# Performance work log

Measured on AMD Instinct MI355X. Metric: run time of the kernel, lower is better.

The kernel has to match this reference:

```python
import jax, jax.numpy as jnp
import numpy as np

B, S, D_MODEL = 2, 2048, 1024
HEADS = 16
DK = D_MODEL // HEADS  # 64
Q_RANK, RANK = 6, 2
ROPE_BASE = 10000.0


def _xavier(key, shape):
    # torch nn.init.xavier_uniform_ on weight (out,in); stored here as (in,out)
    fan_in, fan_out = shape
    a = (6.0 / (fan_in + fan_out)) ** 0.5
    return jax.random.uniform(key, shape, jnp.float32, -a, a)


def setup_inputs() -> dict:
    key = jax.random.key(0)
    ks = jax.random.split(key, 10)
    inp = {
        "q": jax.random.normal(ks[0], (B, S, D_MODEL), jnp.float32),
        "k": jax.random.normal(ks[1], (B, S, D_MODEL), jnp.float32),
        "v": jax.random.normal(ks[2], (B, S, D_MODEL), jnp.float32),
        # causal mask; mask==0 -> -inf in scores
        "mask": jnp.tril(jnp.ones((S, S), dtype=bool))[None, None],
        "W_Aq": _xavier(ks[3], (D_MODEL, Q_RANK * HEADS)),
        "W_Ak": _xavier(ks[4], (D_MODEL, RANK * HEADS)),
        "W_Av": _xavier(ks[5], (D_MODEL, RANK * HEADS)),
        "W_Bq": _xavier(ks[6], (D_MODEL, Q_RANK * DK)),
        "W_Bk": _xavier(ks[7], (D_MODEL, RANK * DK)),
        "W_Bv": _xavier(ks[8], (D_MODEL, RANK * DK)),
        "Wo": _xavier(ks[9], (D_MODEL, D_MODEL)),
    }
    return inp


def _rotary_cos_sin(seq_len, dim):
    inv_freq = 1.0 / (ROPE_BASE ** (jnp.arange(0, dim, 2, dtype=jnp.float32) / dim))
    freqs = jnp.outer(jnp.arange(seq_len, dtype=jnp.float32), inv_freq)  # [S, dim/2]
    return jnp.cos(freqs)[None, :, None, :], jnp.sin(freqs)[None, :, None, :]


def _apply_rotary(x, cos, sin):
    # x: [B, S, R, dk]; rotate-half style RoPE
    d = x.shape[-1] // 2
    x1, x2 = x[..., :d], x[..., d:]
    return jnp.concatenate([x1 * cos + x2 * sin, -x1 * sin + x2 * cos], axis=-1)


def reference(q, k, v, mask, W_Aq, W_Ak, W_Av, W_Bq, W_Bk, W_Bv, Wo):
    Bn, Sn, D = q.shape
    # low-rank factor projections
    A_q = (q @ W_Aq).reshape(Bn, Sn, HEADS, Q_RANK)
    A_k = (k @ W_Ak).reshape(Bn, Sn, HEADS, RANK)
    A_v = (v @ W_Av).reshape(Bn, Sn, HEADS, RANK)
    B_q = (q @ W_Bq).reshape(Bn, Sn, Q_RANK, DK)
    B_k = (k @ W_Bk).reshape(Bn, Sn, RANK, DK)
    B_v = (v @ W_Bv).reshape(Bn, Sn, RANK, DK)
    cos, sin = _rotary_cos_sin(Sn, DK)
    B_q = _apply_rotary(B_q, cos, sin)
    B_k = _apply_rotary(B_k, cos, sin)
    # reconstruct per-head q/k/v: [B,H,S,dk]
    qh = jnp.einsum("bshr,bsrd->bhsd", A_q, B_q) / Q_RANK
    kh = jnp.einsum("bshr,bsrd->bhsd", A_k, B_k) / RANK
    vh = jnp.einsum("bshr,bsrd->bhsd", A_v, B_v) / RANK
    # NOTE: original divides by d_k (not sqrt(d_k)) -- faithful to source
    score = jnp.einsum("bhqd,bhkd->bhqk", qh, kh) / DK
    score = jnp.where(mask, score, -jnp.inf)
    # dropout is identity (eval / dropout=0.0)
    att = jax.nn.softmax(score, axis=-1)
    out = jnp.einsum("bhqk,bhkd->bqhd", att, vh).reshape(Bn, Sn, D)
    return out @ Wo
```

## Files before the change

kernel.cpp:

```cpp
#include <hip/hip_runtime.h>
#include <hip/hip_bf16.h>


typedef __attribute__((ext_vector_type(8))) short short8;
typedef __attribute__((ext_vector_type(4))) float floatx4;

#define MFMA16(a, b, c) __builtin_amdgcn_mfma_f32_16x16x32_bf16(a, b, c, 0, 0, 0)

__device__ __forceinline__ unsigned short bfbits(float x) {
    __hip_bfloat16 h = __float2bfloat16(x);
    return *(unsigned short*)&h;
}

__device__ __forceinline__ float wsrc(int n, int k,
                                      const float* __restrict__ Aq, const float* __restrict__ Bq,
                                      const float* __restrict__ Ak, const float* __restrict__ Bk,
                                      const float* __restrict__ Av, const float* __restrict__ Bv,
                                      const float* __restrict__ Wo) {
    if (n < 96) return Aq[(size_t)k * 96 + n];
    if (n < 480) return Bq[(size_t)k * 384 + (n - 96)];
    if (n < 512) return 0.f;
    if (n < 544) return Ak[(size_t)k * 32 + (n - 512)];
    if (n < 672) return Bk[(size_t)k * 128 + (n - 544)];
    if (n < 768) return 0.f;
    if (n < 800) return Av[(size_t)k * 32 + (n - 768)];
    if (n < 928) return Bv[(size_t)k * 128 + (n - 800)];
    if (n < 1024) return 0.f;
    return Wo[(size_t)k * 1024 + (n - 1024)];
}

__global__ __launch_bounds__(256) void pack_wT_kernel(const float* __restrict__ Aq,
                                                      const float* __restrict__ Bq,
                                                      const float* __restrict__ Ak,
                                                      const float* __restrict__ Bk,
                                                      const float* __restrict__ Av,
                                                      const float* __restrict__ Bv,
                                                      const float* __restrict__ Wo,
                                                      __hip_bfloat16* __restrict__ outBase) {
    __shared__ float tile[64][65];
    int k0 = blockIdx.x * 64, n0 = blockIdx.y * 64;
    int tid = threadIdx.x;
#pragma unroll
    for (int p = 0; p < 16; ++p) {
        int idx = p * 256 + tid;
        int kl = idx >> 6, nl = idx & 63;
        tile[kl][nl] = wsrc(n0 + nl, k0 + kl, Aq, Bq, Ak, Bk, Av, Bv, Wo);
    }
    __syncthreads();
#pragma unroll
    for (int p = 0; p < 16; ++p) {
        int idx = p * 256 + tid;
        int nl = idx >> 6, kl = idx & 63;
        outBase[(size_t)(n0 + nl) * 1024 + k0 + kl] = __float2bfloat16(tile[kl][nl]);
    }
}

__global__ __launch_bounds__(256) void gemm3_kernel(const float* __restrict__ q,
                                                    const float* __restrict__ k,
                                                    const float* __restrict__ v,
                                                    const __hip_bfloat16* __restrict__ WT,
                                                    float* __restrict__ Pq,
                                                    float* __restrict__ Pk,
                                                    float* __restrict__ Pv) {
    __shared__ __align__(16) __hip_bfloat16 As[128][72];
    __shared__ __align__(16) __hip_bfloat16 Bs[64][72];
    int t = blockIdx.x;
    const float* A; float* C; int N, n0, wrow;
    if (t < 8)       { A = q; C = Pq; N = 512; n0 = t * 64;        wrow = t * 64; }
    else if (t < 12) { A = k; C = Pk; N = 256; n0 = (t - 8) * 64;  wrow = 512 + (t - 8) * 64; }
    else             { A = v; C = Pv; N = 256; n0 = (t - 12) * 64; wrow = 768 + (t - 12) * 64; }
    int m0 = blockIdx.y * 128;
    int tid = threadIdx.x;
    int wave = tid >> 6, lane = tid & 63, quad = lane >> 4, l15 = lane & 15;
    int wm = wave >> 1, wn = wave & 1;
    floatx4 acc[4][2];
#pragma unroll
    for (int mt = 0; mt < 4; ++mt)
#pragma unroll
        for (int nt = 0; nt < 2; ++nt) acc[mt][nt] = (floatx4){0.f, 0.f, 0.f, 0.f};

    for (int k0 = 0; k0 < 1024; k0 += 64) {
#pragma unroll
        for (int pp = 0; pp < 8; ++pp) {
            int idx = pp * 256 + tid;
            int row = idx >> 4, c4 = (idx & 15) * 4;
            float4 av = *(const float4*)(A + (size_t)(m0 + row) * 1024 + k0 + c4);
            ushort4 bv;
            bv.x = bfbits(av.x); bv.y = bfbits(av.y); bv.z = bfbits(av.z); bv.w = bfbits(av.w);
            *(ushort4*)&As[row][c4] = bv;
        }
#pragma unroll
        for (int pp = 0; pp < 2; ++pp) {
            int idx = pp * 256 + tid;
            int row = idx >> 3, c8 = (idx & 7) * 8;
            *(uint4*)&Bs[row][c8] = *(const uint4*)(WT + (size_t)(wrow + row) * 1024 + k0 + c8);
        }
        __syncthreads();
#pragma unroll
        for (int ks = 0; ks < 64; ks += 32) {
            short8 af[4], bf[2];
#pragma unroll
            for (int t2 = 0; t2 < 4; ++t2)
                af[t2] = *(const short8*)&As[wm * 64 + t2 * 16 + l15][ks + quad * 8];
#pragma unroll
            for (int t2 = 0; t2 < 2; ++t2)
                bf[t2] = *(const short8*)&Bs[wn * 32 + t2 * 16 + l15][ks + quad * 8];
#pragma unroll
            for (int mt = 0; mt < 4; ++mt)
#pragma unroll
                for (int nt = 0; nt < 2; ++nt)
                    acc[mt][nt] = MFMA16(af[mt], bf[nt], acc[mt][nt]);
        }
        __syncthreads();
    }
#pragma unroll
    for (int mt = 0; mt < 4; ++mt)
#pragma unroll
        for (int nt = 0; nt < 2; ++nt)
#pragma unroll
            for (int r = 0; r < 4; ++r) {
                int row = m0 + wm * 64 + mt * 16 + quad * 4 + r;
                int col = n0 + wn * 32 + nt * 16 + l15;
                C[(size_t)row * N + col] = acc[mt][nt][r];
            }
}

__global__ __launch_bounds__(256) void gemm_out_kernel(const __hip_bfloat16* __restrict__ A,
                                                       const __hip_bfloat16* __restrict__ BT,
                                                       float* __restrict__ C) {
    __shared__ __align__(16) __hip_bfloat16 As[128][72];
    __shared__ __align__(16) __hip_bfloat16 Bs[64][72];
    int n0 = blockIdx.x * 64, m0 = blockIdx.y * 128;
    int tid = threadIdx.x;
    int wave = tid >> 6, lane = tid & 63, quad = lane >> 4, l15 = lane & 15;
    int wm = wave >> 1, wn = wave & 1;
    floatx4 acc[4][2];
#pragma unroll
    for (int mt = 0; mt < 4; ++mt)
#pragma unroll
        for (int nt = 0; nt < 2; ++nt) acc[mt][nt] = (floatx4){0.f, 0.f, 0.f, 0.f};

    for (int k0 = 0; k0 < 1024; k0 += 64) {
#pragma unroll
        for (int pp = 0; pp < 4; ++pp) {
            int idx = pp * 256 + tid;
            int row = idx >> 3, c8 = (idx & 7) * 8;
            *(uint4*)&As[row][c8] = *(const uint4*)(A + (size_t)(m0 + row) * 1024 + k0 + c8);
        }
#pragma unroll
        for (int pp = 0; pp < 2; ++pp) {
            int idx = pp * 256 + tid;
            int row = idx >> 3, c8 = (idx & 7) * 8;
            *(uint4*)&Bs[row][c8] = *(const uint4*)(BT + (size_t)(n0 + row) * 1024 + k0 + c8);
        }
        __syncthreads();
#pragma unroll
        for (int ks = 0; ks < 64; ks += 32) {
            short8 af[4], bf[2];
#pragma unroll
            for (int t2 = 0; t2 < 4; ++t2)
                af[t2] = *(const short8*)&As[wm * 64 + t2 * 16 + l15][ks + quad * 8];
#pragma unroll
            for (int t2 = 0; t2 < 2; ++t2)
                bf[t2] = *(const short8*)&Bs[wn * 32 + t2 * 16 + l15][ks + quad * 8];
#pragma unroll
            for (int mt = 0; mt < 4; ++mt)
#pragma unroll
                for (int nt = 0; nt < 2; ++nt)
                    acc[mt][nt] = MFMA16(af[mt], bf[nt], acc[mt][nt]);
        }
        __syncthreads();
    }
#pragma unroll
    for (int mt = 0; mt < 4; ++mt)
#pragma unroll
        for (int nt = 0; nt < 2; ++nt)
#pragma unroll
            for (int r = 0; r < 4; ++r) {
                int row = m0 + wm * 64 + mt * 16 + quad * 4 + r;
                int col = n0 + wn * 32 + nt * 16 + l15;
                C[(size_t)row * 1024 + col] = acc[mt][nt][r];
            }
}

__global__ __launch_bounds__(256) void combine_rope_kernel(const float* __restrict__ Pq,
                                                           const float* __restrict__ Pk,
                                                           const float* __restrict__ Pv,
                                                           __hip_bfloat16* __restrict__ qh,
                                                           __hip_bfloat16* __restrict__ kh,
                                                           __hip_bfloat16* __restrict__ vh) {
    int t = blockIdx.x, tid = threadIdx.x;
    int b = t >> 11, s = t & 2047;
    __shared__ float Lq[512], Lk[256], Lv[256];
    for (int i = tid; i < 512; i += 256) Lq[i] = Pq[(size_t)t * 512 + i];
    Lk[tid] = Pk[(size_t)t * 256 + tid];
    Lv[tid] = Pv[(size_t)t * 256 + tid];
    __syncthreads();
    if (tid < 192) {
        int r = tid >> 5, d = tid & 31;
        float inv = __expf(-(float)d * 0.28782313662425576f);
        float rev = (float)s * inv * 0.15915494309189535f;
        rev -= floorf(rev);
        float sn = __builtin_amdgcn_sinf(rev);
        float cs = __builtin_amdgcn_cosf(rev);
        float x1 = Lq[96 + r * 64 + d], x2 = Lq[96 + r * 64 + d + 32];
        Lq[96 + r * 64 + d] = x1 * cs + x2 * sn;
        Lq[96 + r * 64 + d + 32] = -x1 * sn + x2 * cs;
    } else {
        int i2 = tid - 192;
        int r = i2 >> 5, d = i2 & 31;
        float inv = __expf(-(float)d * 0.28782313662425576f);
        float rev = (float)s * inv * 0.15915494309189535f;
        rev -= floorf(rev);
        float sn = __builtin_amdgcn_sinf(rev);
        float cs = __builtin_amdgcn_cosf(rev);
        float x1 = Lk[32 + r * 64 + d], x2 = Lk[32 + r * 64 + d + 32];
        Lk[32 + r * 64 + d] = x1 * cs + x2 * sn;
        Lk[32 + r * 64 + d + 32] = -x1 * sn + x2 * cs;
    }
    __syncthreads();
    const float QSCALE = 1.4426950408889634f / 768.0f;
    int bh0 = b * 16;
    for (int i = tid; i < 1024; i += 256) {
        int h = i >> 6, d = i & 63;
        float aq = 0.f;
#pragma unroll
        for (int r = 0; r < 6; ++r) aq += Lq[h * 6 + r] * Lq[96 + r * 64 + d];
        size_t o = ((size_t)(bh0 + h) * 2048 + s) * 64 + d;
        qh[o] = __float2bfloat16(aq * QSCALE);
        float ak = Lk[h * 2] * Lk[32 + d] + Lk[h * 2 + 1] * Lk[96 + d];
        kh[o] = __float2bfloat16(ak);
        float av = Lv[h * 2] * Lv[32 + d] + Lv[h * 2 + 1] * Lv[96 + d];
        vh[o] = __float2bfloat16(av * 0.5f);
    }
}

__global__ __launch_bounds__(256) void transpose_v_kernel(const __hip_bfloat16* __restrict__ vh,
                                                          __hip_bfloat16* __restrict__ vT) {
    __shared__ __hip_bfloat16 tile[64][65];
    int s0 = blockIdx.x * 64, bh = blockIdx.y;
    int tid = threadIdx.x;
#pragma unroll
    for (int p = 0; p < 16; ++p) {
        int idx = p * 256 + tid;
        int r = idx >> 6, c = idx & 63;
        tile[r][c] = vh[((size_t)bh * 2048 + s0 + r) * 64 + c];
    }
    __syncthreads();
#pragma unroll
    for (int p = 0; p < 16; ++p) {
        int idx = p * 256 + tid;
        int r = idx >> 6, c = idx & 63;
        vT[((size_t)bh * 64 + r) * 2048 + s0 + c] = tile[c][r];
    }
}

__global__ __launch_bounds__(256) void flash_kernel(const __hip_bfloat16* __restrict__ qh,
                                                    const __hip_bfloat16* __restrict__ kh,
                                                    const __hip_bfloat16* __restrict__ vT,
                                                    __hip_bfloat16* __restrict__ att) {
    int lin = blockIdx.x + (blockIdx.y << 4);
    int bh = ((lin & 7) << 2) | ((lin >> 3) & 3);
    int p = 15 - (lin >> 5);
    int tid = threadIdx.x;
    int wave = tid >> 6, lane = tid & 63, quad = lane >> 4, l15 = lane & 15;
    int q0 = p * 128;
    __shared__ __align__(16) __hip_bfloat16 Ks[64][72];
    __shared__ __align__(16) __hip_bfloat16 Vts[64][72];
    __shared__ __align__(16) __hip_bfloat16 Ps[4][32][72];

    short8 aq[2][2];
#pragma unroll
    for (int m = 0; m < 2; ++m) {
        const __hip_bfloat16* qrow =
            qh + ((size_t)bh * 2048 + q0 + wave * 32 + m * 16 + l15) * 64 + quad * 8;
        aq[m][0] = *(const short8*)(qrow);
        aq[m][1] = *(const short8*)(qrow + 32);
    }

    floatx4 o[2][4];
#pragma unroll
    for (int m = 0; m < 2; ++m)
#pragma unroll
        for (int nt = 0; nt < 4; ++nt) o[m][nt] = (floatx4){0.f, 0.f, 0.f, 0.f};
    float rs[2][4] = {{0.f, 0.f, 0.f, 0.f}, {0.f, 0.f, 0.f, 0.f}};

    int jmax = 2 * p + 1;
    for (int j = 0; j <= jmax; ++j) {
        int k0 = j * 64;
#pragma unroll
        for (int pp = 0; pp < 2; ++pp) {
            int idx = pp * 256 + tid;
            int row = idx >> 3, c8 = (idx & 7) * 8;
            *(uint4*)&Ks[row][c8] = *(const uint4*)(kh + ((size_t)bh * 2048 + k0 + row) * 64 + c8);
            *(uint4*)&Vts[row][c8] = *(const uint4*)(vT + ((size_t)bh * 64 + row) * 2048 + k0 + c8);
        }
        __syncthreads();

        int krel = j - 2 * p;
        bool skip0 = (krel == 1) && (wave * 32 < 64);
        bool skip1 = (krel == 1) && (wave * 32 + 16 < 64);

        floatx4 s[2][4];
#pragma unroll
        for (int m = 0; m < 2; ++m)
#pragma unroll
            for (int nt = 0; nt < 4; ++nt) s[m][nt] = (floatx4){0.f, 0.f, 0.f, 0.f};
#pragma unroll
        for (int nt = 0; nt < 4; ++nt) {
            short8 bk0 = *(const short8*)&Ks[nt * 16 + l15][quad * 8];
            short8 bk1 = *(const short8*)&Ks[nt * 16 + l15][32 + quad * 8];
            if (!skip0) {
                s[0][nt] = MFMA16(aq[0][0], bk0, s[0][nt]);
                s[0][nt] = MFMA16(aq[0][1], bk1, s[0][nt]);
            }
            if (!skip1) {
                s[1][nt] = MFMA16(aq[1][0], bk0, s[1][nt]);
                s[1][nt] = MFMA16(aq[1][1], bk1, s[1][nt]);
            }
        }
#pragma unroll
        for (int m = 0; m < 2; ++m) {
            bool skip = m == 0 ? skip0 : skip1;
            if (skip) continue;
            int sbase = wave * 32 + m * 16;
            bool domask = (krel >= 0) && (krel * 64 + 63 > sbase);
            if (domask) {
#pragma unroll
                for (int nt = 0; nt < 4; ++nt) {
                    int kcol = k0 + nt * 16 + l15;
#pragma unroll
                    for (int r = 0; r < 4; ++r)
                        if (kcol > q0 + sbase + quad * 4 + r) s[m][nt][r] = -__builtin_inff();
                }
            }
#pragma unroll
            for (int nt = 0; nt < 4; ++nt)
#pragma unroll
                for (int r = 0; r < 4; ++r) {
                    float pe = exp2f(s[m][nt][r]);
                    rs[m][r] += pe;
                    Ps[wave][m * 16 + quad * 4 + r][nt * 16 + l15] = __float2bfloat16(pe);
                }
        }
        __builtin_amdgcn_s_waitcnt(0xC07F);
        short8 pa[2][2];
#pragma unroll
        for (int m = 0; m < 2; ++m) {
            pa[m][0] = *(const short8*)&Ps[wave][m * 16 + l15][quad * 8];
            pa[m][1] = *(const short8*)&Ps[wave][m * 16 + l15][32 + quad * 8];
        }
#pragma unroll
        for (int nt = 0; nt < 4; ++nt) {
            short8 bv0 = *(const short8*)&Vts[nt * 16 + l15][quad * 8];
            short8 bv1 = *(const short8*)&Vts[nt * 16 + l15][32 + quad * 8];
            if (!skip0) {
                o[0][nt] = MFMA16(pa[0][0], bv0, o[0][nt]);
                o[0][nt] = MFMA16(pa[0][1], bv1, o[0][nt]);
            }
            if (!skip1) {
                o[1][nt] = MFMA16(pa[1][0], bv0, o[1][nt]);
                o[1][nt] = MFMA16(pa[1][1], bv1, o[1][nt]);
            }
        }
        __syncthreads();
    }
    int b = bh >> 4, h = bh & 15;
#pragma unroll
    for (int m = 0; m < 2; ++m) {
        float l_i[4];
#pragma unroll
        for (int r = 0; r < 4; ++r) {
            float x = rs[m][r];
            x += __shfl_xor(x, 1, 64);
            x += __shfl_xor(x, 2, 64);
            x += __shfl_xor(x, 4, 64);
            x += __shfl_xor(x, 8, 64);
            l_i[r] = x;
        }
        size_t obase = ((size_t)b * 2048 + q0 + wave * 32 + m * 16 + quad * 4) * 1024 + h * 64;
#pragma unroll
        for (int nt = 0; nt < 4; ++nt)
#pragma unroll
            for (int r = 0; r < 4; ++r)
                att[obase + (size_t)r * 1024 + nt * 16 + l15] = __float2bfloat16(o[m][nt][r] / l_i[r]);
    }
}

extern "C" void kernel_launch(void* const* d_in, const int* in_sizes, int n_in,
                              void* d_out, int out_size, void* d_ws, size_t ws_size,
                              hipStream_t stream) {
    const float* q = (const float*)d_in[0];
    const float* k = (const float*)d_in[1];
    const float* v = (const float*)d_in[2];
    const float* W_Aq = (const float*)d_in[4];
    const float* W_Ak = (const float*)d_in[5];
    const float* W_Av = (const float*)d_in[6];
    const float* W_Bq = (const float*)d_in[7];
    const float* W_Bk = (const float*)d_in[8];
    const float* W_Bv = (const float*)d_in[9];
    const float* Wo = (const float*)d_in[10];
    float* out = (float*)d_out;

    char* w = (char*)d_ws;
    __hip_bfloat16* qh = (__hip_bfloat16*)(w + 0);
    __hip_bfloat16* khp = (__hip_bfloat16*)(w + 8388608);
    __hip_bfloat16* vhN = (__hip_bfloat16*)(w + 16777216);
    __hip_bfloat16* WT = (__hip_bfloat16*)(w + 25165824);
    __hip_bfloat16* WoT = (__hip_bfloat16*)(w + 27262976);
    float* Pq = (float*)(w + 29360128);
    float* Pk = (float*)(w + 37748736);
    float* Pv = (float*)(w + 41943040);
    __hip_bfloat16* att = (__hip_bfloat16*)(w + 29360128);
    __hip_bfloat16* vT = (__hip_bfloat16*)(w + 37748736);

    pack_wT_kernel<<<dim3(16, 32), 256, 0, stream>>>(W_Aq, W_Bq, W_Ak, W_Bk, W_Av, W_Bv, Wo, WT);
    gemm3_kernel<<<dim3(16, 32), 256, 0, stream>>>(q, k, v, WT, Pq, Pk, Pv);
    combine_rope_kernel<<<4096, 256, 0, stream>>>(Pq, Pk, Pv, qh, khp, vhN);
    transpose_v_kernel<<<dim3(32, 32), 256, 0, stream>>>(vhN, vT);
    flash_kernel<<<dim3(16, 32), 256, 0, stream>>>(qh, khp, vT, att);
    gemm_out_kernel<<<dim3(16, 32), 256, 0, stream>>>(att, WoT, out);
}
```

Before: 260.0 us.

## Rework pipeline: larger GEMM tiles, bf16 intermediates, fused combine+transpose, leaner flash

Both GEMMs now use 128x128 tiles on a 1D grid with grouped block ordering, and the projection GEMM writes bf16 instead of fp32 intermediates. The combine/RoPE and V-transpose kernels are merged into one kernel that handles 16 tokens per block and writes vT directly. The flash kernel moves to 64-row query tiles, prefetches the next K/V tile into registers, and computes row sums with an MFMA against a ones matrix instead of shuffles. These changes aim to cut intermediate memory traffic and launch count and to improve load balance, at the cost of extra bf16 rounding in the intermediates and fewer blocks (256) in the GEMMs.

```diff
diff --git a/kernel.cpp b/kernel.cpp
--- a/kernel.cpp
+++ b/kernel.cpp
@@ -7,9 +7,13 @@
 
 #define MFMA16(a, b, c) __builtin_amdgcn_mfma_f32_16x16x32_bf16(a, b, c, 0, 0, 0)
 
+__device__ __forceinline__ float b2f(short s) {
+    unsigned int u = ((unsigned int)(unsigned short)s) << 16;
+    float f; __builtin_memcpy(&f, &u, 4); return f;
+}
 __device__ __forceinline__ unsigned short bfbits(float x) {
     __hip_bfloat16 h = __float2bfloat16(x);
-    return *(unsigned short*)&h;
+    unsigned short u; __builtin_memcpy(&u, &h, 2); return u;
 }
 
 __device__ __forceinline__ float wsrc(int n, int k,
@@ -59,25 +63,26 @@
                                                     const float* __restrict__ k,
                                                     const float* __restrict__ v,
                                                     const __hip_bfloat16* __restrict__ WT,
-                                                    float* __restrict__ Pq,
-                                                    float* __restrict__ Pk,
-                                                    float* __restrict__ Pv) {
+                                                    __hip_bfloat16* __restrict__ Pq,
+                                                    __hip_bfloat16* __restrict__ Pk,
+                                                    __hip_bfloat16* __restrict__ Pv) {
     __shared__ __align__(16) __hip_bfloat16 As[128][72];
-    __shared__ __align__(16) __hip_bfloat16 Bs[64][72];
-    int t = blockIdx.x;
-    const float* A; float* C; int N, n0, wrow;
-    if (t < 8)       { A = q; C = Pq; N = 512; n0 = t * 64;        wrow = t * 64; }
-    else if (t < 12) { A = k; C = Pk; N = 256; n0 = (t - 8) * 64;  wrow = 512 + (t - 8) * 64; }
-    else             { A = v; C = Pv; N = 256; n0 = (t - 12) * 64; wrow = 768 + (t - 12) * 64; }
-    int m0 = blockIdx.y * 128;
+    __shared__ __align__(16) __hip_bfloat16 Bs[128][72];
+    int lin = blockIdx.x;
+    int t = (lin >> 3) & 7;
+    int m0 = ((lin & 7) + ((lin >> 6) << 3)) * 128;
+    const float* A; __hip_bfloat16* C; int N, n0, wrow;
+    if (t < 4)      { A = q; C = Pq; N = 512; n0 = t * 128;        wrow = t * 128; }
+    else if (t < 6) { A = k; C = Pk; N = 256; n0 = (t - 4) * 128;  wrow = 512 + (t - 4) * 128; }
+    else            { A = v; C = Pv; N = 256; n0 = (t - 6) * 128;  wrow = 768 + (t - 6) * 128; }
     int tid = threadIdx.x;
     int wave = tid >> 6, lane = tid & 63, quad = lane >> 4, l15 = lane & 15;
     int wm = wave >> 1, wn = wave & 1;
-    floatx4 acc[4][2];
+    floatx4 acc[4][4];
 #pragma unroll
     for (int mt = 0; mt < 4; ++mt)
 #pragma unroll
-        for (int nt = 0; nt < 2; ++nt) acc[mt][nt] = (floatx4){0.f, 0.f, 0.f, 0.f};
+        for (int nt = 0; nt < 4; ++nt) acc[mt][nt] = (floatx4){0.f, 0.f, 0.f, 0.f};
 
     for (int k0 = 0; k0 < 1024; k0 += 64) {
 #pragma unroll
@@ -90,7 +95,7 @@
             *(ushort4*)&As[row][c4] = bv;
         }
 #pragma unroll
-        for (int pp = 0; pp < 2; ++pp) {
+        for (int pp = 0; pp < 4; ++pp) {
             int idx = pp * 256 + tid;
             int row = idx >> 3, c8 = (idx & 7) * 8;
             *(uint4*)&Bs[row][c8] = *(const uint4*)(WT + (size_t)(wrow + row) * 1024 + k0 + c8);
@@ -98,17 +103,16 @@
         __syncthreads();
 #pragma unroll
         for (int ks = 0; ks < 64; ks += 32) {
-            short8 af[4], bf[2];
-#pragma unroll
-            for (int t2 = 0; t2 < 4; ++t2)
+            short8 af[4], bf[4];
+#pragma unroll
+            for (int t2 = 0; t2 < 4; ++t2) {
                 af[t2] = *(const short8*)&As[wm * 64 + t2 * 16 + l15][ks + quad * 8];
-#pragma unroll
-            for (int t2 = 0; t2 < 2; ++t2)
-                bf[t2] = *(const short8*)&Bs[wn * 32 + t2 * 16 + l15][ks + quad * 8];
+                bf[t2] = *(const short8*)&Bs[wn * 64 + t2 * 16 + l15][ks + quad * 8];
+            }
 #pragma unroll
             for (int mt = 0; mt < 4; ++mt)
 #pragma unroll
-                for (int nt = 0; nt < 2; ++nt)
+                for (int nt = 0; nt < 4; ++nt)
                     acc[mt][nt] = MFMA16(af[mt], bf[nt], acc[mt][nt]);
         }
         __syncthreads();
@@ -116,12 +120,12 @@
 #pragma unroll
     for (int mt = 0; mt < 4; ++mt)
 #pragma unroll
-        for (int nt = 0; nt < 2; ++nt)
+        for (int nt = 0; nt < 4; ++nt)
 #pragma unroll
             for (int r = 0; r < 4; ++r) {
                 int row = m0 + wm * 64 + mt * 16 + quad * 4 + r;
-                int col = n0 + wn * 32 + nt * 16 + l15;
-                C[(size_t)row * N + col] = acc[mt][nt][r];
+                int col = n0 + wn * 64 + nt * 16 + l15;
+                C[(size_t)row * N + col] = __float2bfloat16(acc[mt][nt][r]);
             }
 }
 
@@ -129,16 +133,18 @@
                                                        const __hip_bfloat16* __restrict__ BT,
                                                        float* __restrict__ C) {
     __shared__ __align__(16) __hip_bfloat16 As[128][72];
-    __shared__ __align__(16) __hip_bfloat16 Bs[64][72];
-    int n0 = blockIdx.x * 64, m0 = blockIdx.y * 128;
+    __shared__ __align__(16) __hip_bfloat16 Bs[128][72];
+    int lin = blockIdx.x;
+    int n0 = ((lin >> 3) & 7) * 128;
+    int m0 = ((lin & 7) + ((lin >> 6) << 3)) * 128;
     int tid = threadIdx.x;
     int wave = tid >> 6, lane = tid & 63, quad = lane >> 4, l15 = lane & 15;
     int wm = wave >> 1, wn = wave & 1;
-    floatx4 acc[4][2];
+    floatx4 acc[4][4];
 #pragma unroll
     for (int mt = 0; mt < 4; ++mt)
 #pragma unroll
-        for (int nt = 0; nt < 2; ++nt) acc[mt][nt] = (floatx4){0.f, 0.f, 0.f, 0.f};
+        for (int nt = 0; nt < 4; ++nt) acc[mt][nt] = (floatx4){0.f, 0.f, 0.f, 0.f};
 
     for (int k0 = 0; k0 < 1024; k0 += 64) {
 #pragma unroll
@@ -146,27 +152,21 @@
             int idx = pp * 256 + tid;
             int row = idx >> 3, c8 = (idx & 7) * 8;
             *(uint4*)&As[row][c8] = *(const uint4*)(A + (size_t)(m0 + row) * 1024 + k0 + c8);
-        }
-#pragma unroll
-        for (int pp = 0; pp < 2; ++pp) {
-            int idx = pp * 256 + tid;
-            int row = idx >> 3, c8 = (idx & 7) * 8;
             *(uint4*)&Bs[row][c8] = *(const uint4*)(BT + (size_t)(n0 + row) * 1024 + k0 + c8);
         }
         __syncthreads();
 #pragma unroll
         for (int ks = 0; ks < 64; ks += 32) {
-            short8 af[4], bf[2];
-#pragma unroll
-            for (int t2 = 0; t2 < 4; ++t2)
+            short8 af[4], bf[4];
+#pragma unroll
+            for (int t2 = 0; t2 < 4; ++t2) {
                 af[t2] = *(const short8*)&As[wm * 64 + t2 * 16 + l15][ks + quad * 8];
-#pragma unroll
-            for (int t2 = 0; t2 < 2; ++t2)
-                bf[t2] = *(const short8*)&Bs[wn * 32 + t2 * 16 + l15][ks + quad * 8];
+                bf[t2] = *(const short8*)&Bs[wn * 64 + t2 * 16 + l15][ks + quad * 8];
+            }
 #pragma unroll
             for (int mt = 0; mt < 4; ++mt)
 #pragma unroll
-                for (int nt = 0; nt < 2; ++nt)
+                for (int nt = 0; nt < 4; ++nt)
                     acc[mt][nt] = MFMA16(af[mt], bf[nt], acc[mt][nt]);
         }
         __syncthreads();
@@ -174,84 +174,110 @@
 #pragma unroll
     for (int mt = 0; mt < 4; ++mt)
 #pragma unroll
-        for (int nt = 0; nt < 2; ++nt)
+        for (int nt = 0; nt < 4; ++nt)
 #pragma unroll
             for (int r = 0; r < 4; ++r) {
                 int row = m0 + wm * 64 + mt * 16 + quad * 4 + r;
-                int col = n0 + wn * 32 + nt * 16 + l15;
+                int col = n0 + wn * 64 + nt * 16 + l15;
                 C[(size_t)row * 1024 + col] = acc[mt][nt][r];
             }
 }
 
-__global__ __launch_bounds__(256) void combine_rope_kernel(const float* __restrict__ Pq,
-                                                           const float* __restrict__ Pk,
-                                                           const float* __restrict__ Pv,
-                                                           __hip_bfloat16* __restrict__ qh,
-                                                           __hip_bfloat16* __restrict__ kh,
-                                                           __hip_bfloat16* __restrict__ vh) {
-    int t = blockIdx.x, tid = threadIdx.x;
-    int b = t >> 11, s = t & 2047;
-    __shared__ float Lq[512], Lk[256], Lv[256];
-    for (int i = tid; i < 512; i += 256) Lq[i] = Pq[(size_t)t * 512 + i];
-    Lk[tid] = Pk[(size_t)t * 256 + tid];
-    Lv[tid] = Pv[(size_t)t * 256 + tid];
+__global__ __launch_bounds__(256) void combine_vt_kernel(const __hip_bfloat16* __restrict__ Pq,
+                                                         const __hip_bfloat16* __restrict__ Pk,
+                                                         const __hip_bfloat16* __restrict__ Pv,
+                                                         __hip_bfloat16* __restrict__ qh,
+                                                         __hip_bfloat16* __restrict__ kh,
+                                                         __hip_bfloat16* __restrict__ vT) {
+    __shared__ __align__(16) __hip_bfloat16 LAq[16][96];
+    __shared__ __align__(16) __hip_bfloat16 LAk[16][32];
+    __shared__ __align__(16) __hip_bfloat16 LAv[16][32];
+    __shared__ __align__(16) __hip_bfloat16 LBq[16][6][72];
+    __shared__ __align__(16) __hip_bfloat16 LBk[16][2][72];
+    __shared__ __align__(16) __hip_bfloat16 LBv[16][2][72];
+    int tid = threadIdx.x;
+    int token0 = blockIdx.x * 16;
+    int b = token0 >> 11, s0 = token0 & 2047, bh0 = b * 16;
+
+    for (int i = tid; i < 16 * 512; i += 256) {
+        int s = i >> 9, c = i & 511;
+        __hip_bfloat16 val = Pq[(size_t)(token0 + s) * 512 + c];
+        if (c < 96) LAq[s][c] = val;
+        else if (c < 480) LBq[s][(c - 96) >> 6][(c - 96) & 63] = val;
+    }
+    for (int i = tid; i < 16 * 256; i += 256) {
+        int s = i >> 8, c = i & 255;
+        __hip_bfloat16 vk = Pk[(size_t)(token0 + s) * 256 + c];
+        __hip_bfloat16 vv = Pv[(size_t)(token0 + s) * 256 + c];
+        if (c < 32) { LAk[s][c] = vk; LAv[s][c] = vv; }
+        else if (c < 160) {
+            LBk[s][(c - 32) >> 6][(c - 32) & 63] = vk;
+            LBv[s][(c - 32) >> 6][(c - 32) & 63] = vv;
+        }
+    }
     __syncthreads();
-    if (tid < 192) {
-        int r = tid >> 5, d = tid & 31;
+    for (int i = tid; i < 4096; i += 256) {
+        int s = i >> 8, rr = (i >> 5) & 7, d = i & 31;
         float inv = __expf(-(float)d * 0.28782313662425576f);
-        float rev = (float)s * inv * 0.15915494309189535f;
+        float rev = (float)(s0 + s) * inv * 0.15915494309189535f;
         rev -= floorf(rev);
         float sn = __builtin_amdgcn_sinf(rev);
         float cs = __builtin_amdgcn_cosf(rev);
-        float x1 = Lq[96 + r * 64 + d], x2 = Lq[96 + r * 64 + d + 32];
-        Lq[96 + r * 64 + d] = x1 * cs + x2 * sn;
-        Lq[96 + r * 64 + d + 32] = -x1 * sn + x2 * cs;
-    } else {
-        int i2 = tid - 192;
-        int r = i2 >> 5, d = i2 & 31;
-        float inv = __expf(-(float)d * 0.28782313662425576f);
-        float rev = (float)s * inv * 0.15915494309189535f;
-        rev -= floorf(rev);
-        float sn = __builtin_amdgcn_sinf(rev);
-        float cs = __builtin_amdgcn_cosf(rev);
-        float x1 = Lk[32 + r * 64 + d], x2 = Lk[32 + r * 64 + d + 32];
-        Lk[32 + r * 64 + d] = x1 * cs + x2 * sn;
-        Lk[32 + r * 64 + d + 32] = -x1 * sn + x2 * cs;
+        if (rr < 6) {
+            float x1 = b2f(*(short*)&LBq[s][rr][d]), x2 = b2f(*(short*)&LBq[s][rr][d + 32]);
+            LBq[s][rr][d] = __float2bfloat16(x1 * cs + x2 * sn);
+            LBq[s][rr][d + 32] = __float2bfloat16(-x1 * sn + x2 * cs);
+        } else {
+            int r2 = rr - 6;
+            float x1 = b2f(*(short*)&LBk[s][r2][d]), x2 = b2f(*(short*)&LBk[s][r2][d + 32]);
+            LBk[s][r2][d] = __float2bfloat16(x1 * cs + x2 * sn);
+            LBk[s][r2][d + 32] = __float2bfloat16(-x1 * sn + x2 * cs);
+        }
     }
     __syncthreads();
     const float QSCALE = 1.4426950408889634f / 768.0f;
-    int bh0 = b * 16;
-    for (int i = tid; i < 1024; i += 256) {
-        int h = i >> 6, d = i & 63;
-        float aq = 0.f;
-#pragma unroll
-        for (int r = 0; r < 6; ++r) aq += Lq[h * 6 + r] * Lq[96 + r * 64 + d];
-        size_t o = ((size_t)(bh0 + h) * 2048 + s) * 64 + d;
-        qh[o] = __float2bfloat16(aq * QSCALE);
-        float ak = Lk[h * 2] * Lk[32 + d] + Lk[h * 2 + 1] * Lk[96 + d];
-        kh[o] = __float2bfloat16(ak);
-        float av = Lv[h * 2] * Lv[32 + d] + Lv[h * 2 + 1] * Lv[96 + d];
-        vh[o] = __float2bfloat16(av * 0.5f);
-    }
-}
-
-__global__ __launch_bounds__(256) void transpose_v_kernel(const __hip_bfloat16* __restrict__ vh,
-                                                          __hip_bfloat16* __restrict__ vT) {
-    __shared__ __hip_bfloat16 tile[64][65];
-    int s0 = blockIdx.x * 64, bh = blockIdx.y;
-    int tid = threadIdx.x;
-#pragma unroll
-    for (int p = 0; p < 16; ++p) {
-        int idx = p * 256 + tid;
-        int r = idx >> 6, c = idx & 63;
-        tile[r][c] = vh[((size_t)bh * 2048 + s0 + r) * 64 + c];
-    }
-    __syncthreads();
-#pragma unroll
-    for (int p = 0; p < 16; ++p) {
-        int idx = p * 256 + tid;
-        int r = idx >> 6, c = idx & 63;
-        vT[((size_t)bh * 64 + r) * 2048 + s0 + c] = tile[c][r];
+    {
+        int s = tid >> 4, h = tid & 15;
+        float aq[6], ak0, ak1;
+#pragma unroll
+        for (int r = 0; r < 6; ++r) aq[r] = b2f(*(short*)&LAq[s][h * 6 + r]);
+        ak0 = b2f(*(short*)&LAk[s][h * 2]);
+        ak1 = b2f(*(short*)&LAk[s][h * 2 + 1]);
+        size_t obase = ((size_t)(bh0 + h) * 2048 + s0 + s) * 64;
+#pragma unroll
+        for (int dc = 0; dc < 64; dc += 8) {
+            float accq[8] = {0, 0, 0, 0, 0, 0, 0, 0};
+#pragma unroll
+            for (int r = 0; r < 6; ++r) {
+                short8 bq = *(const short8*)&LBq[s][r][dc];
+#pragma unroll
+                for (int e = 0; e < 8; ++e) accq[e] += aq[r] * b2f(bq[e]);
+            }
+            short8 bk0 = *(const short8*)&LBk[s][0][dc];
+            short8 bk1 = *(const short8*)&LBk[s][1][dc];
+            ushort outq[8], outk[8];
+#pragma unroll
+            for (int e = 0; e < 8; ++e) {
+                outq[e] = bfbits(accq[e] * QSCALE);
+                outk[e] = bfbits(ak0 * b2f(bk0[e]) + ak1 * b2f(bk1[e]));
+            }
+            *(uint4*)((__hip_bfloat16*)qh + obase + dc) = *(uint4*)outq;
+            *(uint4*)((__hip_bfloat16*)kh + obase + dc) = *(uint4*)outk;
+        }
+    }
+    {
+        int s = tid & 15, dg = tid >> 4;
+#pragma unroll
+        for (int h = 0; h < 16; ++h) {
+            float a0 = b2f(*(short*)&LAv[s][h * 2]) * 0.5f;
+            float a1 = b2f(*(short*)&LAv[s][h * 2 + 1]) * 0.5f;
+#pragma unroll
+            for (int dd = 0; dd < 4; ++dd) {
+                int d = dg * 4 + dd;
+                float val = a0 * b2f(*(short*)&LBv[s][0][d]) + a1 * b2f(*(short*)&LBv[s][1][d]);
+                vT[((size_t)(bh0 + h) * 64 + d) * 2048 + s0 + s] = __float2bfloat16(val);
+            }
+        }
     }
 }
 
@@ -259,132 +285,114 @@
                                                     const __hip_bfloat16* __restrict__ kh,
                                                     const __hip_bfloat16* __restrict__ vT,
                                                     __hip_bfloat16* __restrict__ att) {
-    int lin = blockIdx.x + (blockIdx.y << 4);
+    int lin = blockIdx.x + (blockIdx.y << 5);
     int bh = ((lin & 7) << 2) | ((lin >> 3) & 3);
-    int p = 15 - (lin >> 5);
+    int qi = 31 - (lin >> 5);
     int tid = threadIdx.x;
     int wave = tid >> 6, lane = tid & 63, quad = lane >> 4, l15 = lane & 15;
-    int q0 = p * 128;
+    int q0 = qi * 64;
     __shared__ __align__(16) __hip_bfloat16 Ks[64][72];
     __shared__ __align__(16) __hip_bfloat16 Vts[64][72];
-    __shared__ __align__(16) __hip_bfloat16 Ps[4][32][72];
-
-    short8 aq[2][2];
-#pragma unroll
-    for (int m = 0; m < 2; ++m) {
-        const __hip_bfloat16* qrow =
-            qh + ((size_t)bh * 2048 + q0 + wave * 32 + m * 16 + l15) * 64 + quad * 8;
-        aq[m][0] = *(const short8*)(qrow);
-        aq[m][1] = *(const short8*)(qrow + 32);
-    }
-
-    floatx4 o[2][4];
-#pragma unroll
-    for (int m = 0; m < 2; ++m)
-#pragma unroll
-        for (int nt = 0; nt < 4; ++nt) o[m][nt] = (floatx4){0.f, 0.f, 0.f, 0.f};
-    float rs[2][4] = {{0.f, 0.f, 0.f, 0.f}, {0.f, 0.f, 0.f, 0.f}};
-
-    int jmax = 2 * p + 1;
-    for (int j = 0; j <= jmax; ++j) {
-        int k0 = j * 64;
+    __shared__ __align__(16) __hip_bfloat16 Ps[4][16][72];
+    __shared__ __align__(16) __hip_bfloat16 Ones[16][72];
+
+    {
+        __hip_bfloat16* of = (__hip_bfloat16*)Ones;
+        for (int i = tid; i < 16 * 72; i += 256)
+            of[i] = __float2bfloat16(i < 72 ? 1.f : 0.f);
+    }
+    __syncthreads();
+    short8 ones0 = *(const short8*)&Ones[l15][quad * 8];
+    short8 ones1 = *(const short8*)&Ones[l15][32 + quad * 8];
+
+    const __hip_bfloat16* qrow = qh + ((size_t)bh * 2048 + q0 + wave * 16 + l15) * 64 + quad * 8;
+    short8 aq0 = *(const short8*)(qrow);
+    short8 aq1 = *(const short8*)(qrow + 32);
+
+    floatx4 o[4];
+#pragma unroll
+    for (int nt = 0; nt < 4; ++nt) o[nt] = (floatx4){0.f, 0.f, 0.f, 0.f};
+    floatx4 ls = (floatx4){0.f, 0.f, 0.f, 0.f};
+
+    uint4 kreg[2], vreg[2];
+#pragma unroll
+    for (int pp = 0; pp < 2; ++pp) {
+        int idx = pp * 256 + tid;
+        int row = idx >> 3, c8 = (idx & 7) * 8;
+        kreg[pp] = *(const uint4*)(kh + ((size_t)bh * 2048 + row) * 64 + c8);
+        vreg[pp] = *(const uint4*)(vT + ((size_t)bh * 64 + row) * 2048 + c8);
+    }
+
+    for (int j = 0; j <= qi; ++j) {
+        if (j) __syncthreads();
 #pragma unroll
         for (int pp = 0; pp < 2; ++pp) {
             int idx = pp * 256 + tid;
             int row = idx >> 3, c8 = (idx & 7) * 8;
-            *(uint4*)&Ks[row][c8] = *(const uint4*)(kh + ((size_t)bh * 2048 + k0 + row) * 64 + c8);
-            *(uint4*)&Vts[row][c8] = *(const uint4*)(vT + ((size_t)bh * 64 + row) * 2048 + k0 + c8);
+            *(uint4*)&Ks[row][c8] = kreg[pp];
+            *(uint4*)&Vts[row][c8] = vreg[pp];
+        }
+        if (j < qi) {
+            int k0n = (j + 1) * 64;
+#pragma unroll
+            for (int pp = 0; pp < 2; ++pp) {
+                int idx = pp * 256 + tid;
+                int row = idx >> 3, c8 = (idx & 7) * 8;
+                kreg[pp] = *(const uint4*)(kh + ((size_t)bh * 2048 + k0n + row) * 64 + c8);
+                vreg[pp] = *(const uint4*)(vT + ((size_t)bh * 64 + row) * 2048 + k0n + c8);
+            }
         }
         __syncthreads();
 
-        int krel = j - 2 * p;
-        bool skip0 = (krel == 1) && (wave * 32 < 64);
-        bool skip1 = (krel == 1) && (wave * 32 + 16 < 64);
-
-        floatx4 s[2][4];
-#pragma unroll
-        for (int m = 0; m < 2; ++m)
-#pragma unroll
-            for (int nt = 0; nt < 4; ++nt) s[m][nt] = (floatx4){0.f, 0.f, 0.f, 0.f};
+        floatx4 s[4];
+#pragma unroll
+        for (int nt = 0; nt < 4; ++nt) s[nt] = (floatx4){0.f, 0.f, 0.f, 0.f};
 #pragma unroll
         for (int nt = 0; nt < 4; ++nt) {
             short8 bk0 = *(const short8*)&Ks[nt * 16 + l15][quad * 8];
             short8 bk1 = *(const short8*)&Ks[nt * 16 + l15][32 + quad * 8];
-            if (!skip0) {
-                s[0][nt] = MFMA16(aq[0][0], bk0, s[0][nt]);
-                s[0][nt] = MFMA16(aq[0][1], bk1, s[0][nt]);
-            }
-            if (!skip1) {
-                s[1][nt] = MFMA16(aq[1][0], bk0, s[1][nt]);
-                s[1][nt] = MFMA16(aq[1][1], bk1, s[1][nt]);
-            }
-        }
-#pragma unroll
-        for (int m = 0; m < 2; ++m) {
-            bool skip = m == 0 ? skip0 : skip1;
-            if (skip) continue;
-            int sbase = wave * 32 + m * 16;
-            bool domask = (krel >= 0) && (krel * 64 + 63 > sbase);
-            if (domask) {
-#pragma unroll
-                for (int nt = 0; nt < 4; ++nt) {
-                    int kcol = k0 + nt * 16 + l15;
-#pragma unroll
-                    for (int r = 0; r < 4; ++r)
-                        if (kcol > q0 + sbase + quad * 4 + r) s[m][nt][r] = -__builtin_inff();
-                }
-            }
-#pragma unroll
-            for (int nt = 0; nt < 4; ++nt)
-#pragma unroll
-                for (int r = 0; r < 4; ++r) {
-                    float pe = exp2f(s[m][nt][r]);
-                    rs[m][r] += pe;
-                    Ps[wave][m * 16 + quad * 4 + r][nt * 16 + l15] = __float2bfloat16(pe);
-                }
-        }
+            s[nt] = MFMA16(aq0, bk0, s[nt]);
+            s[nt] = MFMA16(aq1, bk1, s[nt]);
+        }
+        if (j == qi) {
+            int rbase = wave * 16 + quad * 4;
+#pragma unroll
+            for (int nt = 0; nt < 4; ++nt) {
+                int cl = nt * 16 + l15;
+#pragma unroll
+                for (int r = 0; r < 4; ++r)
+                    if (cl > rbase + r) s[nt][r] = -__builtin_inff();
+            }
+        }
+#pragma unroll
+        for (int nt = 0; nt < 4; ++nt)
+#pragma unroll
+            for (int r = 0; r < 4; ++r)
+                Ps[wave][quad * 4 + r][nt * 16 + l15] = __float2bfloat16(exp2f(s[nt][r]));
         __builtin_amdgcn_s_waitcnt(0xC07F);
-        short8 pa[2][2];
-#pragma unroll
-        for (int m = 0; m < 2; ++m) {
-            pa[m][0] = *(const short8*)&Ps[wave][m * 16 + l15][quad * 8];
-            pa[m][1] = *(const short8*)&Ps[wave][m * 16 + l15][32 + quad * 8];
-        }
+        short8 pa0 = *(const short8*)&Ps[wave][l15][quad * 8];
+        short8 pa1 = *(const short8*)&Ps[wave][l15][32 + quad * 8];
+        ls = MFMA16(pa0, ones0, ls);
+        ls = MFMA16(pa1, ones1, ls);
 #pragma unroll
         for (int nt = 0; nt < 4; ++nt) {
             short8 bv0 = *(const short8*)&Vts[nt * 16 + l15][quad * 8];
             short8 bv1 = *(const short8*)&Vts[nt * 16 + l15][32 + quad * 8];
-            if (!skip0) {
-                o[0][nt] = MFMA16(pa[0][0], bv0, o[0][nt]);
-                o[0][nt] = MFMA16(pa[0][1], bv1, o[0][nt]);
-            }
-            if (!skip1) {
-                o[1][nt] = MFMA16(pa[1][0], bv0, o[1][nt]);
-                o[1][nt] = MFMA16(pa[1][1], bv1, o[1][nt]);
-            }
-        }
-        __syncthreads();
-    }
+            o[nt] = MFMA16(pa0, bv0, o[nt]);
+            o[nt] = MFMA16(pa1, bv1, o[nt]);
+        }
+    }
+    float inv_l[4];
+#pragma unroll
+    for (int r = 0; r < 4; ++r)
+        inv_l[r] = 1.0f / __shfl(ls[r], lane & 48, 64);
     int b = bh >> 4, h = bh & 15;
-#pragma unroll
-    for (int m = 0; m < 2; ++m) {
-        float l_i[4];
-#pragma unroll
-        for (int r = 0; r < 4; ++r) {
-            float x = rs[m][r];
-            x += __shfl_xor(x, 1, 64);
-            x += __shfl_xor(x, 2, 64);
-            x += __shfl_xor(x, 4, 64);
-            x += __shfl_xor(x, 8, 64);
-            l_i[r] = x;
-        }
-        size_t obase = ((size_t)b * 2048 + q0 + wave * 32 + m * 16 + quad * 4) * 1024 + h * 64;
-#pragma unroll
-        for (int nt = 0; nt < 4; ++nt)
-#pragma unroll
-            for (int r = 0; r < 4; ++r)
-                att[obase + (size_t)r * 1024 + nt * 16 + l15] = __float2bfloat16(o[m][nt][r] / l_i[r]);
-    }
+    size_t obase = ((size_t)b * 2048 + q0 + wave * 16 + quad * 4) * 1024 + h * 64;
+#pragma unroll
+    for (int nt = 0; nt < 4; ++nt)
+#pragma unroll
+        for (int r = 0; r < 4; ++r)
+            att[obase + (size_t)r * 1024 + nt * 16 + l15] = __float2bfloat16(o[nt][r] * inv_l[r]);
 }
 
 extern "C" void kernel_launch(void* const* d_in, const int* in_sizes, int n_in,
@@ -403,21 +411,19 @@
     float* out = (float*)d_out;
 
     char* w = (char*)d_ws;
-    __hip_bfloat16* qh = (__hip_bfloat16*)(w + 0);
-    __hip_bfloat16* khp = (__hip_bfloat16*)(w + 8388608);
-    __hip_bfloat16* vhN = (__hip_bfloat16*)(w + 16777216);
-    __hip_bfloat16* WT = (__hip_bfloat16*)(w + 25165824);
-    __hip_bfloat16* WoT = (__hip_bfloat16*)(w + 27262976);
-    float* Pq = (float*)(w + 29360128);
-    float* Pk = (float*)(w + 37748736);
-    float* Pv = (float*)(w + 41943040);
-    __hip_bfloat16* att = (__hip_bfloat16*)(w + 29360128);
-    __hip_bfloat16* vT = (__hip_bfloat16*)(w + 37748736);
+    __hip_bfloat16* qh  = (__hip_bfloat16*)(w + 0);
+    __hip_bfloat16* kh  = (__hip_bfloat16*)(w + 8388608);
+    __hip_bfloat16* vT  = (__hip_bfloat16*)(w + 16777216);
+    __hip_bfloat16* WT  = (__hip_bfloat16*)(w + 25165824);
+    __hip_bfloat16* WoT = WT + (size_t)1024 * 1024;
+    __hip_bfloat16* Pq  = (__hip_bfloat16*)(w + 29360128);
+    __hip_bfloat16* Pk  = (__hip_bfloat16*)(w + 33554432);
+    __hip_bfloat16* Pv  = (__hip_bfloat16*)(w + 35651584);
+    __hip_bfloat16* att = (__hip_bfloat16*)(w + 37748736);
 
     pack_wT_kernel<<<dim3(16, 32), 256, 0, stream>>>(W_Aq, W_Bq, W_Ak, W_Bk, W_Av, W_Bv, Wo, WT);
-    gemm3_kernel<<<dim3(16, 32), 256, 0, stream>>>(q, k, v, WT, Pq, Pk, Pv);
-    combine_rope_kernel<<<4096, 256, 0, stream>>>(Pq, Pk, Pv, qh, khp, vhN);
-    transpose_v_kernel<<<dim3(32, 32), 256, 0, stream>>>(vhN, vT);
-    flash_kernel<<<dim3(16, 32), 256, 0, stream>>>(qh, khp, vT, att);
-    gemm_out_kernel<<<dim3(16, 32), 256, 0, stream>>>(att, WoT, out);
-}
+    gemm3_kernel<<<256, 256, 0, stream>>>(q, k, v, WT, Pq, Pk, Pv);
+    combine_vt_kernel<<<256, 256, 0, stream>>>(Pq, Pk, Pv, qh, kh, vT);
+    flash_kernel<<<dim3(32, 32), 256, 0, stream>>>(qh, kh, vT, att);
+    gemm_out_kernel<<<256, 256, 0, stream>>>(att, WoT, out);
+}
```

After: 287.3 us. 10.5% more time.
